# Optimization experiments

Measured on AMD Instinct MI355X. Metric: run time of the kernel, lower is better.

The kernel has to match this reference:

```python
import jax, jax.numpy as jnp
import numpy as np

B, LINES, NREG, D, L, K, CATS = 256, 64, 64, 1024, 64, 16, 2
EPS = 1e-5

_idx = np.arange(K)
# modular digit-wise add / sub mixing tables: M[i,j,m] = 1 iff (i op j) mod K == m
M_ADD = jnp.asarray(((_idx[:, None] + _idx[None, :]) % K)[..., None] == _idx[None, None, :], dtype=jnp.float32)
M_SUB = jnp.asarray(((_idx[:, None] - _idx[None, :]) % K)[..., None] == _idx[None, None, :], dtype=jnp.float32)


def _ln(x, g, b):
    m = x.mean(-1, keepdims=True)
    v = ((x - m) ** 2).mean(-1, keepdims=True)
    return (x - m) / jnp.sqrt(v + EPS) * g + b


def setup_inputs() -> dict:
    key = jax.random.key(0)
    ks = jax.random.split(key, 12)
    p = jax.random.uniform(ks[0], (B, LINES, CATS))
    opcode_probs = p / p.sum(-1, keepdims=True)
    registers = jax.random.normal(ks[1], (B, NREG, D))
    k_write = jax.random.normal(ks[2], (B, LINES, D))
    q_read = jax.random.normal(ks[3], (B, LINES, 2, D))
    cond_distribution = jax.random.uniform(ks[4], (B, LINES, 4))
    gate = jax.random.uniform(ks[5], (B, LINES, 1))
    s = 0.02
    F = L * K
    return {
        'opcode_probs': opcode_probs, 'registers': registers, 'k_write': k_write,
        'q_read': q_read, 'cond_distribution': cond_distribution, 'gate': gate,
        'ln1_g': jnp.ones((D,)), 'ln1_b': jnp.zeros((D,)),
        'w1': jax.random.normal(ks[6], (D, F)) * s, 'b1': jnp.zeros((F,)),
        'ln2_g': jnp.ones((D,)), 'ln2_b': jnp.zeros((D,)),
        'w2': jax.random.normal(ks[7], (D, F)) * s, 'b2': jnp.zeros((F,)),
        'w_res': jax.random.normal(ks[8], (F, D)) * s, 'b_res': jnp.zeros((D,)),
        'lno_g': jnp.ones((D,)), 'lno_b': jnp.zeros((D,)),
    }


def reference(opcode_probs, registers, k_write, q_read, cond_distribution, gate,
              ln1_g, ln1_b, w1, b1, ln2_g, ln2_b, w2, b2, w_res, b_res, lno_g, lno_b):
    scale = 1.0 / jnp.sqrt(jnp.asarray(D, jnp.float32))

    def digit_op(x, y, M):
        # x,y: (b,l,k) digit distributions -> (b,l,k) modular arithmetic result
        return jnp.einsum('bli,blj,ijm->blm', x, y, M)

    def step(R, xs):
        prob, q, kw, g = xs  # (b,2) (b,2,d) (b,d) (b,1)
        # attention read of two operands from register memory
        attn = jax.nn.softmax(jnp.einsum('bqd,brd->bqr', q, R) * scale, axis=-1)
        op_s = jnp.einsum('bqr,brd->bqd', attn, R)
        x = jax.nn.softmax((_ln(op_s[:, 0], ln1_g, ln1_b) @ w1 + b1).reshape(-1, L, K), axis=-1)
        y = jax.nn.softmax((_ln(op_s[:, 1], ln2_g, ln2_b) @ w2 + b2).reshape(-1, L, K), axis=-1)
        outs = jnp.stack([digit_op(x, y, M_ADD), digit_op(x, y, M_SUB)], axis=1)  # (b,2,l,k)
        mix = jnp.einsum('bn,bnlk->blk', prob, outs).reshape(-1, L * K)
        value = _ln(mix @ w_res + b_res, lno_g, lno_b)  # (b,d)
        # attention write-back with gate
        w = jax.nn.softmax(jnp.einsum('bd,brd->br', kw, R) * scale, axis=-1)
        gw = (g * w)[..., None]  # (b,r,1)
        R = R * (1.0 - gw) + gw * value[:, None, :]
        return R, None

    xs = (jnp.moveaxis(opcode_probs, 1, 0), jnp.moveaxis(q_read, 1, 0),
          jnp.moveaxis(k_write, 1, 0), jnp.moveaxis(gate, 1, 0))
    R, _ = jax.lax.scan(step, registers, xs)
    return R
```

## Files before the change

kernel.cpp:

```cpp
#include <hip/hip_runtime.h>
#include <hip/hip_bf16.h>

#define BB 256
#define LINES 64
#define NREG 64
#define DD 1024
#define FF 1024

constexpr float EPS = 1e-5f;
constexpr float SCALE = 0.03125f;

typedef __bf16 bf16_t;
typedef bf16_t bf16x8 __attribute__((ext_vector_type(8)));
typedef unsigned short us16x8 __attribute__((ext_vector_type(8)));
typedef float f32x4 __attribute__((ext_vector_type(4)));
typedef unsigned long long u64;

#define WS_W1T   0u
#define WS_W2T   (2u << 20)
#define WS_WRT   (4u << 20)
#define WS_XNP   (6u << 20)
#define WS_GT    ((7u << 20) + (1u << 19))
#define WS_CTR   ((8u << 20) + (1u << 19))
#define WS_XCDC  (WS_CTR + 1024u)
#define WS_NEED  (WS_XCDC + 64u)

#define SM_WV    0
#define SM_AT0P  256
#define SM_AT1P  512
#define SM_SC0   768
#define SM_SC1   1024
#define SM_SCW   1280
#define SM_RED   1536
#define SM_DYNID 1792
#define SM_DYN   2048
#define SM_OSB   SM_DYN
#define SM_AT0   SM_DYN
#define SM_AT1   (SM_DYN + 32768)
#define SM_RED2  (SM_DYN + 65536)
#define SM_PRE   (SM_DYN + 65536 + 13056)
#define SM_VAL   (SM_DYN + 65536 + 13056 + 8448)
#define SM_QPF   (SM_VAL + 4352)
#define SM_MIXT  (SM_QPF + 15360)
#define SM_SIZE  (SM_MIXT + 2304)

__device__ __forceinline__ float wred(float v) {
#pragma unroll
  for (int m = 32; m >= 1; m >>= 1) v += __shfl_xor(v, m);
  return v;
}
__device__ __forceinline__ float wmax64(float v) {
#pragma unroll
  for (int m = 32; m >= 1; m >>= 1) v = fmaxf(v, __shfl_xor(v, m));
  return v;
}

__device__ __forceinline__ void st_llc32(void* p, unsigned v) {
  asm volatile("global_store_dword %0, %1, off sc0 sc1" :: "v"(p), "v"(v) : "memory");
}
__device__ __forceinline__ unsigned ld_llc32(const void* p) {
  unsigned r;
  asm volatile("global_load_dword %0, %1, off sc0 sc1\n\ts_waitcnt vmcnt(0)"
               : "=v"(r) : "v"(p) : "memory");
  return r;
}
__device__ __forceinline__ void ld_llc_4x8_nw(const void* p, u64& a, u64& b, u64& c, u64& d) {
  asm volatile(
      "global_load_dwordx2 %0, %4, off sc0 sc1\n\t"
      "global_load_dwordx2 %1, %4, off offset:8 sc0 sc1\n\t"
      "global_load_dwordx2 %2, %4, off offset:16 sc0 sc1\n\t"
      "global_load_dwordx2 %3, %4, off offset:24 sc0 sc1"
      : "=&v"(a), "=&v"(b), "=&v"(c), "=&v"(d) : "v"(p) : "memory");
}
__device__ __forceinline__ void wait_vm0() {
  asm volatile("s_waitcnt vmcnt(0)" ::: "memory");
  __builtin_amdgcn_sched_barrier(0);
}

__device__ __forceinline__ void group_barrier(unsigned* flg, int tid, int m, unsigned tag) {
  asm volatile("s_waitcnt vmcnt(0)" ::: "memory");
  __syncthreads();
  if (tid < 64) {
    if (tid == 0) st_llc32(&flg[m], tag);
    for (;;) {
      unsigned v = (tid < 16) ? ld_llc32(&flg[tid]) : tag;
      if (__all(v >= tag)) break;
      __builtin_amdgcn_s_sleep(2);
    }
  }
  __syncthreads();
}

__global__ __launch_bounds__(256) void transcvt(const float* __restrict__ w1,
                                                const float* __restrict__ w2,
                                                const float* __restrict__ wr,
                                                bf16_t* __restrict__ out) {
  __shared__ float tl[64][65];
  const float* src = (blockIdx.z == 0) ? w1 : (blockIdx.z == 1) ? w2 : wr;
  bf16_t* dst = out + (size_t)blockIdx.z * (1u << 20);
  const int i0 = blockIdx.x * 64, j0 = blockIdx.y * 64;
  const int t = threadIdx.x;
#pragma unroll
  for (int it = 0; it < 4; ++it) {
    int r = (t >> 4) + it * 16;
    int c4 = (t & 15) * 4;
    const float4 v = *reinterpret_cast<const float4*>(&src[(size_t)(i0 + r) * 1024 + j0 + c4]);
    tl[r][c4] = v.x; tl[r][c4 + 1] = v.y; tl[r][c4 + 2] = v.z; tl[r][c4 + 3] = v.w;
  }
  __syncthreads();
  const int orow = t >> 2, seg = t & 3;
  bf16x8 v0, v1;
#pragma unroll
  for (int u = 0; u < 8; ++u) {
    v0[u] = (bf16_t)tl[seg * 16 + u][orow];
    v1[u] = (bf16_t)tl[seg * 16 + 8 + u][orow];
  }
  bf16_t* dp = dst + (size_t)(j0 + orow) * 1024 + i0 + seg * 16;
  *reinterpret_cast<bf16x8*>(dp) = v0;
  *reinterpret_cast<bf16x8*>(dp + 8) = v1;
}

__global__ __launch_bounds__(1024, 4) void interp5(
    const float* __restrict__ opcode_probs, const float* __restrict__ Rin,
    const float* __restrict__ k_write, const float* __restrict__ q_read,
    const float* __restrict__ gate,
    const float* __restrict__ ln1_g, const float* __restrict__ ln1_b, const float* __restrict__ b1,
    const float* __restrict__ ln2_g, const float* __restrict__ ln2_b, const float* __restrict__ b2,
    const float* __restrict__ b_res, const float* __restrict__ lno_g, const float* __restrict__ lno_b,
    char* __restrict__ ws, float* __restrict__ Rout) {
  __shared__ __align__(16) char smem[SM_SIZE];
  float* wvp  = (float*)(smem + SM_WV);
  float* at0p = (float*)(smem + SM_AT0P);
  float* at1p = (float*)(smem + SM_AT1P);
  float* sc0p = (float*)(smem + SM_SC0);
  float* sc1p = (float*)(smem + SM_SC1);
  float* scwp = (float*)(smem + SM_SCW);
  float* redp = (float*)(smem + SM_RED);
  int*   dyn  = (int*)(smem + SM_DYNID);

  const int tid = threadIdx.x;
  const int w = tid >> 6, lane = tid & 63;
  const int ln15 = lane & 15, kgrp = lane >> 4;

  if (tid == 0) {
    unsigned x = __builtin_amdgcn_s_getreg(20 | (31 << 11)) & 7;
    unsigned r = atomicAdd((unsigned*)(ws + WS_XCDC) + x, 1u);
    dyn[0] = (int)x; dyn[1] = (int)r;
  }
  __syncthreads();
  const int xcd = dyn[0];
  const int rnk = dyn[1];
  const int g = (rnk >> 1) & 15;
  const int m = ((xcd << 1) | (rnk & 1)) & 15;
  const int j = m;
  const int bq = g * 16 + j;

  const bf16_t* w1t = (const bf16_t*)(ws + WS_W1T);
  const bf16_t* w2t = (const bf16_t*)(ws + WS_W2T);
  const bf16_t* wrt = (const bf16_t*)(ws + WS_WRT);
  unsigned* xnp   = (unsigned*)(ws + WS_XNP);
  float*    gtf   = (float*)(ws + WS_GT);
  unsigned* gtu   = (unsigned*)(ws + WS_GT);
  unsigned* flg   = (unsigned*)(ws + WS_CTR) + g * 16;

  float Rr_[4][16];
  {
    const float* Rsrc = Rin + (size_t)bq * (NREG * DD);
#pragma unroll
    for (int rr = 0; rr < 4; ++rr) {
#pragma unroll
      for (int c = 0; c < 4; ++c) {
        float4 v = *(const float4*)(Rsrc + (size_t)(4 * w + rr) * DD + lane * 16 + c * 4);
        Rr_[rr][c * 4 + 0] = v.x; Rr_[rr][c * 4 + 1] = v.y;
        Rr_[rr][c * 4 + 2] = v.z; Rr_[rr][c * 4 + 3] = v.w;
      }
    }
  }

  {
    const float* qb = q_read + ((size_t)bq * LINES + 0) * (2 * DD);
    const float* kb = k_write + ((size_t)bq * LINES + 0) * DD;
    float* qpf = (float*)(smem + SM_QPF);
    const int pidx = (tid >> 4) * 20 + (tid & 15);
    qpf[pidx] = qb[tid];
    qpf[1280 + pidx] = qb[DD + tid];
    qpf[2560 + pidx] = kb[tid];
  }
  __syncthreads();

  unsigned nbar = 0;

  for (int t = 0; t < LINES; ++t) {
    {
      const float* qpf = (const float*)(smem + SM_QPF);
      const int pb = lane * 20;
#pragma unroll
      for (int v = 0; v < 3; ++v) {
        float* dst = (v == 0) ? sc0p : (v == 1) ? sc1p : scwp;
        float qv[16];
#pragma unroll
        for (int c = 0; c < 4; ++c) {
          float4 t4 = *(const float4*)(qpf + v * 1280 + pb + c * 4);
          qv[c * 4 + 0] = t4.x; qv[c * 4 + 1] = t4.y;
          qv[c * 4 + 2] = t4.z; qv[c * 4 + 3] = t4.w;
        }
#pragma unroll
        for (int rr = 0; rr < 4; ++rr) {
          float s = 0.f;
#pragma unroll
          for (int jj = 0; jj < 16; ++jj) s = fmaf(Rr_[rr][jj], qv[jj], s);
          s = wred(s);
          if (lane == 0) dst[4 * w + rr] = s * SCALE;
        }
      }
    }
    __syncthreads();
    if (w < 3) {
      const float* src = (w == 0) ? sc0p : (w == 1) ? sc1p : scwp;
      float* dst = (w == 0) ? at0p : (w == 1) ? at1p : wvp;
      float v = src[lane];
      float mx = wmax64(v);
      float e = expf(v - mx);
      float s = wred(e);
      dst[lane] = e / s;
    }
    float pf0, pf1, pf2;
    {
      int tn = (t + 1 < LINES) ? (t + 1) : (LINES - 1);
      const float* qb2 = q_read + ((size_t)bq * LINES + tn) * (2 * DD);
      const float* kb2 = k_write + ((size_t)bq * LINES + tn) * DD;
      pf0 = qb2[tid]; pf1 = qb2[DD + tid]; pf2 = kb2[tid];
    }
    __syncthreads();
    float os0, os1;
    {
      float p0[16], p1[16];
#pragma unroll
      for (int jj = 0; jj < 16; ++jj) { p0[jj] = 0.f; p1[jj] = 0.f; }
#pragma unroll
      for (int rr = 0; rr < 4; ++rr) {
        float a0 = at0p[4 * w + rr], a1 = at1p[4 * w + rr];
#pragma unroll
        for (int jj = 0; jj < 16; ++jj) {
          p0[jj] = fmaf(a0, Rr_[rr][jj], p0[jj]);
          p1[jj] = fmaf(a1, Rr_[rr][jj], p1[jj]);
        }
      }
      float* osb = (float*)(smem + SM_OSB);
      const int rp = (tid >> 4) * 17 + (tid & 15);
#pragma unroll
      for (int jj = 0; jj < 16; ++jj) osb[w * 1088 + lane * 17 + jj] = p0[jj];
      __syncthreads();
      os0 = 0.f;
#pragma unroll
      for (int ww = 0; ww < 16; ++ww) os0 += osb[ww * 1088 + rp];
      __syncthreads();
#pragma unroll
      for (int jj = 0; jj < 16; ++jj) osb[w * 1088 + lane * 17 + jj] = p1[jj];
      __syncthreads();
      os1 = 0.f;
#pragma unroll
      for (int ww = 0; ww < 16; ++ww) os1 += osb[ww * 1088 + rp];
    }
    {
      float s0 = wred(os0), qq0 = wred(os0 * os0);
      float s1 = wred(os1), qq1 = wred(os1 * os1);
      if (lane == 0) { redp[w*4] = s0; redp[w*4+1] = qq0; redp[w*4+2] = s1; redp[w*4+3] = qq1; }
      __syncthreads();
      float S0 = 0, Q0 = 0, S1 = 0, Q1 = 0;
#pragma unroll
      for (int i = 0; i < 16; ++i) { S0 += redp[i*4]; Q0 += redp[i*4+1]; S1 += redp[i*4+2]; Q1 += redp[i*4+3]; }
      float m0 = S0 * (1.f / DD), v0 = fmaxf(Q0 * (1.f / DD) - m0 * m0, 0.f);
      float m1 = S1 * (1.f / DD), v1 = fmaxf(Q1 * (1.f / DD) - m1 * m1, 0.f);
      float xn0v = (os0 - m0) * rsqrtf(v0 + EPS) * ln1_g[tid] + ln1_b[tid];
      float xn1v = (os1 - m1) * rsqrtf(v1 + EPS) * ln2_g[tid] + ln2_b[tid];
      unsigned pw = (unsigned)__builtin_bit_cast(unsigned short, (bf16_t)xn0v)
                  | ((unsigned)__builtin_bit_cast(unsigned short, (bf16_t)xn1v) << 16);
      st_llc32(&xnp[((size_t)g * 16 + j) * DD + tid], pw);
    }
    group_barrier(flg, tid, m, ++nbar);

    {
      const char* base = (const char*)(xnp + (size_t)g * (16 * DD));
      const int row = tid >> 7, k16 = tid & 127;
      u64 a0, a1, a2, a3, c0, c1, c2, c3;
      ld_llc_4x8_nw(base + (size_t)row * 4096 + k16 * 32, a0, a1, a2, a3);
      ld_llc_4x8_nw(base + (size_t)(row + 8) * 4096 + k16 * 32, c0, c1, c2, c3);
      wait_vm0();
#pragma unroll
      for (int h = 0; h < 2; ++h) {
        u64 x0 = h ? c0 : a0, x1 = h ? c1 : a1, x2 = h ? c2 : a2, x3 = h ? c3 : a3;
        int r = row + h * 8;
        us16x8 v0, v1;
        v0[0] = (unsigned short)x0;         v1[0] = (unsigned short)(x0 >> 16);
        v0[1] = (unsigned short)(x0 >> 32); v1[1] = (unsigned short)(x0 >> 48);
        v0[2] = (unsigned short)x1;         v1[2] = (unsigned short)(x1 >> 16);
        v0[3] = (unsigned short)(x1 >> 32); v1[3] = (unsigned short)(x1 >> 48);
        v0[4] = (unsigned short)x2;         v1[4] = (unsigned short)(x2 >> 16);
        v0[5] = (unsigned short)(x2 >> 32); v1[5] = (unsigned short)(x2 >> 48);
        v0[6] = (unsigned short)x3;         v1[6] = (unsigned short)(x3 >> 16);
        v0[7] = (unsigned short)(x3 >> 32); v1[7] = (unsigned short)(x3 >> 48);
        unsigned byte = (unsigned)(r * 2048 + k16 * 16) ^ ((unsigned)(r & 7) << 4);
        *(us16x8*)(smem + SM_AT0 + byte) = v0;
        *(us16x8*)(smem + SM_AT1 + byte) = v1;
      }
    }
    __syncthreads();

#pragma unroll
    for (int gm = 0; gm < 2; ++gm) {
      const char* atile = smem + (gm ? SM_AT1 : SM_AT0);
      const int ns = w & 3, ks = w >> 2;
      const bf16_t* bsrc = (gm ? w2t : w1t) + (size_t)(64 * m + ns * 16 + ln15) * DD;
      f32x4 acc = {0.f, 0.f, 0.f, 0.f};
#pragma unroll
      for (int kc = 0; kc < 8; ++kc) {
        int kb = ks * 256 + kc * 32 + kgrp * 8;
        unsigned abyte = ((unsigned)(ln15 * 2048 + kb * 2)) ^ ((unsigned)(ln15 & 7) << 4);
        bf16x8 av = *(const bf16x8*)(atile + abyte);
        bf16x8 bv = *(const bf16x8*)(bsrc + kb);
        acc = __builtin_amdgcn_mfma_f32_16x16x32_bf16(av, bv, acc, 0, 0, 0);
      }
      float* red2 = (float*)(smem + SM_RED2);
      if (ks > 0) {
#pragma unroll
        for (int r2 = 0; r2 < 4; ++r2)
          red2[((ks - 1) * 4 + ns) * (16 * 17) + (kgrp * 4 + r2) * 17 + ln15] = acc[r2];
      }
      __syncthreads();
      if (ks == 0) {
        float* prep = (float*)(smem + SM_PRE) + gm * (16 * 66);
#pragma unroll
        for (int r2 = 0; r2 < 4; ++r2) {
          int crow = kgrp * 4 + r2;
          float v = acc[r2];
#pragma unroll
          for (int kk = 0; kk < 3; ++kk)
            v += red2[(kk * 4 + ns) * (16 * 17) + crow * 17 + ln15];
          prep[crow * 66 + ns * 16 + ln15] = v;
        }
      }
      __syncthreads();
    }
    {
      float* prep = (float*)(smem + SM_PRE);
      const int bb2 = w, c = lane;
      float xp = prep[bb2 * 66 + c] + b1[64 * m + c];
      float yp = prep[16 * 66 + bb2 * 66 + c] + b2[64 * m + c];
      float mx1 = xp, mx2 = yp;
#pragma unroll
      for (int msk = 1; msk < 16; msk <<= 1) {
        mx1 = fmaxf(mx1, __shfl_xor(mx1, msk));
        mx2 = fmaxf(mx2, __shfl_xor(mx2, msk));
      }
      float e1 = expf(xp - mx1), e2 = expf(yp - mx2);
      float s1 = e1, s2 = e2;
#pragma unroll
      for (int msk = 1; msk < 16; msk <<= 1) {
        s1 += __shfl_xor(s1, msk);
        s2 += __shfl_xor(s2, msk);
      }
      float x = e1 / s1, y = e2 / s2;
      int mm = lane & 15, basel = lane & ~15;
      float addv = 0.f, subv = 0.f;
#pragma unroll
      for (int i = 0; i < 16; ++i) {
        float xi = __shfl(x, basel + i);
        float ya = __shfl(y, basel + ((mm - i) & 15));
        float ys = __shfl(y, basel + ((i - mm) & 15));
        addv = fmaf(xi, ya, addv);
        subv = fmaf(xi, ys, subv);
      }
      int q2 = g * 16 + bb2;
      const float* pr = opcode_probs + ((size_t)q2 * LINES + t) * 2;
      float mix = pr[0] * addv + pr[1] * subv;
      ((bf16_t*)(smem + SM_MIXT))[bb2 * 72 + c] = (bf16_t)mix;
    }
    __syncthreads();

    {
      const bf16_t* mixT = (const bf16_t*)(smem + SM_MIXT);
      f32x4 acc[4] = {{0.f,0.f,0.f,0.f},{0.f,0.f,0.f,0.f},{0.f,0.f,0.f,0.f},{0.f,0.f,0.f,0.f}};
#pragma unroll
      for (int ks2 = 0; ks2 < 2; ++ks2) {
        int fk = ks2 * 32 + kgrp * 8;
        bf16x8 av = *(const bf16x8*)(mixT + ln15 * 72 + fk);
#pragma unroll
        for (int nt2 = 0; nt2 < 4; ++nt2) {
          int d = 64 * w + nt2 * 16 + ln15;
          const bf16_t* bp = wrt + (size_t)d * DD + 64 * m + fk;
          bf16x8 bv = *(const bf16x8*)bp;
          acc[nt2] = __builtin_amdgcn_mfma_f32_16x16x32_bf16(av, bv, acc[nt2], 0, 0, 0);
        }
      }
#pragma unroll
      for (int nt2 = 0; nt2 < 4; ++nt2) {
        int d = 64 * w + nt2 * 16 + ln15;
#pragma unroll
        for (int r2 = 0; r2 < 4; ++r2) {
          int crow = kgrp * 4 + r2;
          atomicAdd(&gtf[((size_t)g * 16 + crow) * DD + d], acc[nt2][r2]);
        }
      }
    }
    group_barrier(flg, tid, m, ++nbar);

    {
      float xv = __builtin_bit_cast(float, ld_llc32(&gtu[((size_t)g * 16 + j) * DD + tid]))
               + b_res[tid];
      st_llc32(&gtu[((size_t)g * 16 + j) * DD + tid], 0u);
      float s1 = wred(xv), s2 = wred(xv * xv);
      if (lane == 0) { redp[w * 2] = s1; redp[w * 2 + 1] = s2; }
      __syncthreads();
      float S = 0.f, Q = 0.f;
#pragma unroll
      for (int i = 0; i < 16; ++i) { S += redp[i * 2]; Q += redp[i * 2 + 1]; }
      float mn = S * (1.f / DD), vr = fmaxf(Q * (1.f / DD) - mn * mn, 0.f);
      float vv = (xv - mn) * rsqrtf(vr + EPS) * lno_g[tid] + lno_b[tid];
      float* valp = (float*)(smem + SM_VAL);
      valp[(tid >> 4) * 17 + (tid & 15)] = vv;
    }
    __syncthreads();
    {
      float gtv = gate[(size_t)bq * LINES + t];
      const float* valp = (const float*)(smem + SM_VAL);
      float vvj[16];
#pragma unroll
      for (int jj = 0; jj < 16; ++jj) vvj[jj] = valp[lane * 17 + jj];
#pragma unroll
      for (int rr = 0; rr < 4; ++rr) {
        float gg = gtv * wvp[4 * w + rr];
#pragma unroll
        for (int jj = 0; jj < 16; ++jj)
          Rr_[rr][jj] = Rr_[rr][jj] * (1.f - gg) + gg * vvj[jj];
      }
      float* qpf = (float*)(smem + SM_QPF);
      const int pidx = (tid >> 4) * 20 + (tid & 15);
      qpf[pidx] = pf0;
      qpf[1280 + pidx] = pf1;
      qpf[2560 + pidx] = pf2;
    }
    __syncthreads();
  }

  {
    float* Rdst = Rout + (size_t)bq * (NREG * DD);
#pragma unroll
    for (int rr = 0; rr < 4; ++rr) {
#pragma unroll
      for (int c = 0; c < 4; ++c) {
        float4 v;
        v.x = Rr_[rr][c * 4 + 0]; v.y = Rr_[rr][c * 4 + 1];
        v.z = Rr_[rr][c * 4 + 2]; v.w = Rr_[rr][c * 4 + 3];
        *(float4*)(Rdst + (size_t)(4 * w + rr) * DD + lane * 16 + c * 4) = v;
      }
    }
  }
}

__global__ __launch_bounds__(1024) void interp_fb(
    const float* __restrict__ opcode_probs, const float* __restrict__ k_write,
    const float* __restrict__ q_read, const float* __restrict__ gate,
    const float* __restrict__ ln1_g, const float* __restrict__ ln1_b,
    const float* __restrict__ w1, const float* __restrict__ b1,
    const float* __restrict__ ln2_g, const float* __restrict__ ln2_b,
    const float* __restrict__ w2, const float* __restrict__ b2,
    const float* __restrict__ w_res, const float* __restrict__ b_res,
    const float* __restrict__ lno_g, const float* __restrict__ lno_b,
    float* __restrict__ R) {
  __shared__ float q0s[DD], q1s[DD], kws[DD];
  __shared__ float sc0[NREG], sc1[NREG], scw[NREG];
  __shared__ float at0[NREG], at1[NREG], wv[NREG];
  __shared__ float xn0[DD], xn1[DD];
  __shared__ float mixs[FF];
  __shared__ float val[DD];
  __shared__ float red[64];
  const int b = blockIdx.x;
  const int tid = threadIdx.x;
  const int w = tid >> 6, lane = tid & 63;
  float* Rb = R + (size_t)b * NREG * DD;
  for (int t = 0; t < LINES; ++t) {
    const float* qb = q_read + ((size_t)b * LINES + t) * 2 * DD;
    const float* kb = k_write + ((size_t)b * LINES + t) * DD;
    q0s[tid] = qb[tid]; q1s[tid] = qb[DD + tid]; kws[tid] = kb[tid];
    __syncthreads();
#pragma unroll
    for (int rr = 0; rr < 4; ++rr) {
      int r = w * 4 + rr;
      const float* Rr = Rb + (size_t)r * DD;
      float a0 = 0.f, a1 = 0.f, aw = 0.f;
#pragma unroll
      for (int jj = 0; jj < 16; ++jj) {
        int d = jj * 64 + lane;
        float rv = Rr[d];
        a0 += rv * q0s[d]; a1 += rv * q1s[d]; aw += rv * kws[d];
      }
      a0 = wred(a0); a1 = wred(a1); aw = wred(aw);
      if (lane == 0) { sc0[r] = a0 * SCALE; sc1[r] = a1 * SCALE; scw[r] = aw * SCALE; }
    }
    __syncthreads();
    if (w < 3) {
      const float* src = (w == 0) ? sc0 : (w == 1) ? sc1 : scw;
      float* dst = (w == 0) ? at0 : (w == 1) ? at1 : wv;
      float v = src[lane];
      float mx = wmax64(v);
      float e = expf(v - mx);
      float s = wred(e);
      dst[lane] = e / s;
    }
    __syncthreads();
    float os0 = 0.f, os1 = 0.f;
#pragma unroll 4
    for (int r = 0; r < NREG; ++r) {
      float rv = Rb[(size_t)r * DD + tid];
      os0 += at0[r] * rv; os1 += at1[r] * rv;
    }
    {
      float s0 = wred(os0), qq0 = wred(os0 * os0);
      float s1 = wred(os1), qq1 = wred(os1 * os1);
      if (lane == 0) { red[w*4] = s0; red[w*4+1] = qq0; red[w*4+2] = s1; red[w*4+3] = qq1; }
      __syncthreads();
      float S0 = 0, Q0 = 0, S1 = 0, Q1 = 0;
#pragma unroll
      for (int i = 0; i < 16; ++i) { S0 += red[i*4]; Q0 += red[i*4+1]; S1 += red[i*4+2]; Q1 += red[i*4+3]; }
      float m0 = S0 / DD, v0 = fmaxf(Q0 / DD - m0 * m0, 0.f);
      float m1 = S1 / DD, v1 = fmaxf(Q1 / DD - m1 * m1, 0.f);
      xn0[tid] = (os0 - m0) * rsqrtf(v0 + EPS) * ln1_g[tid] + ln1_b[tid];
      xn1[tid] = (os1 - m1) * rsqrtf(v1 + EPS) * ln2_g[tid] + ln2_b[tid];
      __syncthreads();
    }
    float p1v = b1[tid], p2v = b2[tid];
    {
      const float* c1 = w1 + tid;
      const float* c2 = w2 + tid;
#pragma unroll 4
      for (int d = 0; d < DD; ++d) {
        p1v += xn0[d] * c1[(size_t)d * FF];
        p2v += xn1[d] * c2[(size_t)d * FF];
      }
    }
    {
      int mmm = lane & 15, basel = lane & ~15;
      float mx1 = p1v, mx2 = p2v;
      for (int msk = 1; msk < 16; msk <<= 1) {
        mx1 = fmaxf(mx1, __shfl_xor(mx1, msk));
        mx2 = fmaxf(mx2, __shfl_xor(mx2, msk));
      }
      float e1 = expf(p1v - mx1), e2 = expf(p2v - mx2);
      float s1 = e1, s2 = e2;
      for (int msk = 1; msk < 16; msk <<= 1) { s1 += __shfl_xor(s1, msk); s2 += __shfl_xor(s2, msk); }
      float x = e1 / s1, y = e2 / s2;
      float addv = 0.f, subv = 0.f;
#pragma unroll
      for (int i = 0; i < 16; ++i) {
        float xi = __shfl(x, basel + i);
        float ya = __shfl(y, basel + ((mmm - i) & 15));
        float ys = __shfl(y, basel + ((i - mmm) & 15));
        addv += xi * ya; subv += xi * ys;
      }
      const float* pr = opcode_probs + ((size_t)b * LINES + t) * 2;
      mixs[tid] = pr[0] * addv + pr[1] * subv;
    }
    __syncthreads();
    float acc = b_res[tid];
    {
      const float* cr = w_res + tid;
#pragma unroll 4
      for (int f = 0; f < FF; ++f) acc += mixs[f] * cr[(size_t)f * DD];
    }
    {
      float s1 = wred(acc), s2 = wred(acc * acc);
      if (lane == 0) { red[w*2] = s1; red[w*2+1] = s2; }
      __syncthreads();
      float S = 0, Q = 0;
#pragma unroll
      for (int i = 0; i < 16; ++i) { S += red[i*2]; Q += red[i*2+1]; }
      float mn = S / DD, vr = fmaxf(Q / DD - mn * mn, 0.f);
      val[tid] = (acc - mn) * rsqrtf(vr + EPS) * lno_g[tid] + lno_b[tid];
      __syncthreads();
    }
    {
      float gt_ = gate[(size_t)b * LINES + t];
      float vv = val[tid];
#pragma unroll 4
      for (int r = 0; r < NREG; ++r) {
        float gg = gt_ * wv[r];
        size_t idx = (size_t)r * DD + tid;
        Rb[idx] = Rb[idx] * (1.f - gg) + gg * vv;
      }
    }
    __syncthreads();
  }
}

extern "C" void kernel_launch(void* const* d_in, const int* in_sizes, int n_in,
                              void* d_out, int out_size, void* d_ws, size_t ws_size,
                              hipStream_t stream) {
  const float* opcode = (const float*)d_in[0];
  const float* registers = (const float*)d_in[1];
  const float* k_write = (const float*)d_in[2];
  const float* q_read = (const float*)d_in[3];
  const float* gate = (const float*)d_in[5];
  const float* ln1_g = (const float*)d_in[6];
  const float* ln1_b = (const float*)d_in[7];
  const float* w1 = (const float*)d_in[8];
  const float* b1 = (const float*)d_in[9];
  const float* ln2_g = (const float*)d_in[10];
  const float* ln2_b = (const float*)d_in[11];
  const float* w2 = (const float*)d_in[12];
  const float* b2 = (const float*)d_in[13];
  const float* w_res = (const float*)d_in[14];
  const float* b_res = (const float*)d_in[15];
  const float* lno_g = (const float*)d_in[16];
  const float* lno_b = (const float*)d_in[17];
  float* R = (float*)d_out;

  if (ws_size >= (size_t)WS_NEED) {
    transcvt<<<dim3(16, 16, 3), 256, 0, stream>>>(w1, w2, w_res, (bf16_t*)d_ws);
    hipMemsetAsync((char*)d_ws + WS_GT, 0, (1u << 20) + 2048, stream);
    interp5<<<BB, 1024, 0, stream>>>(opcode, registers, k_write, q_read, gate,
                                     ln1_g, ln1_b, b1, ln2_g, ln2_b, b2,
                                     b_res, lno_g, lno_b, (char*)d_ws, R);
  } else {
    hipMemcpyAsync(R, registers, (size_t)BB * NREG * DD * sizeof(float),
                   hipMemcpyDeviceToDevice, stream);
    interp_fb<<<BB, 1024, 0, stream>>>(opcode, k_write, q_read, gate, ln1_g, ln1_b,
                                       w1, b1, ln2_g, ln2_b, w2, b2, w_res, b_res,
                                       lno_g, lno_b, R);
  }
}
```

Measured before the change: 4.126 ms.

## Precompute next-step attention scores before barrier and apply write-back algebraically

The per-step q·R and k·R score dot products now run on the pre-update registers, placed before the group barrier so they overlap the wait. The scores are then corrected algebraically for the gated write-back, using the dot products of q and k with the new value vector and the previous gate weights. The block-to-batch mapping also drops the XCD-based atomic rank assignment in favour of blockIdx directly. This adds a few extra reductions and reorders floating-point arithmetic, and it changes which blocks share the L2-coherent group barrier.

Result: no change. 4.088 ms (-0.9%).

```diff
diff --git a/kernel.cpp b/kernel.cpp
--- a/kernel.cpp
+++ b/kernel.cpp
@@ -22,17 +22,16 @@
 #define WS_XNP   (6u << 20)
 #define WS_GT    ((7u << 20) + (1u << 19))
 #define WS_CTR   ((8u << 20) + (1u << 19))
-#define WS_XCDC  (WS_CTR + 1024u)
-#define WS_NEED  (WS_XCDC + 64u)
+#define WS_NEED  (WS_CTR + 1024u)
 
 #define SM_WV    0
 #define SM_AT0P  256
 #define SM_AT1P  512
-#define SM_SC0   768
-#define SM_SC1   1024
-#define SM_SCW   1280
+#define SM_PC0   768
+#define SM_PC1   1024
+#define SM_PCW   1280
 #define SM_RED   1536
-#define SM_DYNID 1792
+#define SM_VQG   1856
 #define SM_DYN   2048
 #define SM_OSB   SM_DYN
 #define SM_AT0   SM_DYN
@@ -77,11 +76,11 @@
   __builtin_amdgcn_sched_barrier(0);
 }
 
-__device__ __forceinline__ void group_barrier(unsigned* flg, int tid, int m, unsigned tag) {
+__device__ __forceinline__ void group_barrier(unsigned* flg, int tid, int me, unsigned tag) {
   asm volatile("s_waitcnt vmcnt(0)" ::: "memory");
   __syncthreads();
   if (tid < 64) {
-    if (tid == 0) st_llc32(&flg[m], tag);
+    if (tid == 0) st_llc32(&flg[me], tag);
     for (;;) {
       unsigned v = (tid < 16) ? ld_llc32(&flg[tid]) : tag;
       if (__all(v >= tag)) break;
@@ -120,7 +119,7 @@
   *reinterpret_cast<bf16x8*>(dp + 8) = v1;
 }
 
-__global__ __launch_bounds__(1024, 4) void interp5(
+__global__ __launch_bounds__(1024, 4) void interp6(
     const float* __restrict__ opcode_probs, const float* __restrict__ Rin,
     const float* __restrict__ k_write, const float* __restrict__ q_read,
     const float* __restrict__ gate,
@@ -132,28 +131,21 @@
   float* wvp  = (float*)(smem + SM_WV);
   float* at0p = (float*)(smem + SM_AT0P);
   float* at1p = (float*)(smem + SM_AT1P);
-  float* sc0p = (float*)(smem + SM_SC0);
-  float* sc1p = (float*)(smem + SM_SC1);
-  float* scwp = (float*)(smem + SM_SCW);
+  float* pc0  = (float*)(smem + SM_PC0);
+  float* pc1  = (float*)(smem + SM_PC1);
+  float* pcw  = (float*)(smem + SM_PCW);
   float* redp = (float*)(smem + SM_RED);
-  int*   dyn  = (int*)(smem + SM_DYNID);
+  float* vqg  = (float*)(smem + SM_VQG);
 
   const int tid = threadIdx.x;
   const int w = tid >> 6, lane = tid & 63;
   const int ln15 = lane & 15, kgrp = lane >> 4;
 
-  if (tid == 0) {
-    unsigned x = __builtin_amdgcn_s_getreg(20 | (31 << 11)) & 7;
-    unsigned r = atomicAdd((unsigned*)(ws + WS_XCDC) + x, 1u);
-    dyn[0] = (int)x; dyn[1] = (int)r;
-  }
-  __syncthreads();
-  const int xcd = dyn[0];
-  const int rnk = dyn[1];
-  const int g = (rnk >> 1) & 15;
-  const int m = ((xcd << 1) | (rnk & 1)) & 15;
-  const int j = m;
-  const int bq = g * 16 + j;
+  const int b = blockIdx.x;
+  const int g = b >> 4;
+  const int j = b & 15;
+  const int m = ((b & 7) << 1) | ((b >> 3) & 1);
+  const int bq = b;
 
   const bf16_t* w1t = (const bf16_t*)(ws + WS_W1T);
   const bf16_t* w2t = (const bf16_t*)(ws + WS_W2T);
@@ -185,40 +177,43 @@
     qpf[pidx] = qb[tid];
     qpf[1280 + pidx] = qb[DD + tid];
     qpf[2560 + pidx] = kb[tid];
+    if (tid < 64) wvp[tid] = 0.f;
+    if (tid < 4) vqg[tid] = 0.f;
   }
   __syncthreads();
+  {
+    const float* qpf = (const float*)(smem + SM_QPF);
+    const int pb = lane * 20;
+#pragma unroll
+    for (int v = 0; v < 3; ++v) {
+      float* dst = (v == 0) ? pc0 : (v == 1) ? pc1 : pcw;
+      float qv[16];
+#pragma unroll
+      for (int c = 0; c < 4; ++c) {
+        float4 t4 = *(const float4*)(qpf + v * 1280 + pb + c * 4);
+        qv[c * 4 + 0] = t4.x; qv[c * 4 + 1] = t4.y;
+        qv[c * 4 + 2] = t4.z; qv[c * 4 + 3] = t4.w;
+      }
+#pragma unroll
+      for (int rr = 0; rr < 4; ++rr) {
+        float s = 0.f;
+#pragma unroll
+        for (int jj = 0; jj < 16; ++jj) s = fmaf(Rr_[rr][jj], qv[jj], s);
+        s = wred(s);
+        if (lane == 0) dst[4 * w + rr] = s;
+      }
+    }
+  }
+  __syncthreads();
 
   unsigned nbar = 0;
 
   for (int t = 0; t < LINES; ++t) {
-    {
-      const float* qpf = (const float*)(smem + SM_QPF);
-      const int pb = lane * 20;
-#pragma unroll
-      for (int v = 0; v < 3; ++v) {
-        float* dst = (v == 0) ? sc0p : (v == 1) ? sc1p : scwp;
-        float qv[16];
-#pragma unroll
-        for (int c = 0; c < 4; ++c) {
-          float4 t4 = *(const float4*)(qpf + v * 1280 + pb + c * 4);
-          qv[c * 4 + 0] = t4.x; qv[c * 4 + 1] = t4.y;
-          qv[c * 4 + 2] = t4.z; qv[c * 4 + 3] = t4.w;
-        }
-#pragma unroll
-        for (int rr = 0; rr < 4; ++rr) {
-          float s = 0.f;
-#pragma unroll
-          for (int jj = 0; jj < 16; ++jj) s = fmaf(Rr_[rr][jj], qv[jj], s);
-          s = wred(s);
-          if (lane == 0) dst[4 * w + rr] = s * SCALE;
-        }
-      }
-    }
-    __syncthreads();
     if (w < 3) {
-      const float* src = (w == 0) ? sc0p : (w == 1) ? sc1p : scwp;
+      const float* P = (w == 0) ? pc0 : (w == 1) ? pc1 : pcw;
       float* dst = (w == 0) ? at0p : (w == 1) ? at1p : wvp;
-      float v = src[lane];
+      float gw = vqg[3] * wvp[lane];
+      float v = ((1.f - gw) * P[lane] + gw * vqg[w]) * SCALE;
       float mx = wmax64(v);
       float e = expf(v - mx);
       float s = wred(e);
@@ -278,7 +273,7 @@
                   | ((unsigned)__builtin_bit_cast(unsigned short, (bf16_t)xn1v) << 16);
       st_llc32(&xnp[((size_t)g * 16 + j) * DD + tid], pw);
     }
-    group_barrier(flg, tid, m, ++nbar);
+    group_barrier(flg, tid, j, ++nbar);
 
     {
       const char* base = (const char*)(xnp + (size_t)g * (16 * DD));
@@ -403,42 +398,81 @@
         }
       }
     }
-    group_barrier(flg, tid, m, ++nbar);
-
-    {
-      float xv = __builtin_bit_cast(float, ld_llc32(&gtu[((size_t)g * 16 + j) * DD + tid]))
-               + b_res[tid];
-      st_llc32(&gtu[((size_t)g * 16 + j) * DD + tid], 0u);
-      float s1 = wred(xv), s2 = wred(xv * xv);
-      if (lane == 0) { redp[w * 2] = s1; redp[w * 2 + 1] = s2; }
-      __syncthreads();
-      float S = 0.f, Q = 0.f;
-#pragma unroll
-      for (int i = 0; i < 16; ++i) { S += redp[i * 2]; Q += redp[i * 2 + 1]; }
-      float mn = S * (1.f / DD), vr = fmaxf(Q * (1.f / DD) - mn * mn, 0.f);
-      float vv = (xv - mn) * rsqrtf(vr + EPS) * lno_g[tid] + lno_b[tid];
-      float* valp = (float*)(smem + SM_VAL);
-      valp[(tid >> 4) * 17 + (tid & 15)] = vv;
-    }
-    __syncthreads();
-    {
-      float gtv = gate[(size_t)bq * LINES + t];
-      const float* valp = (const float*)(smem + SM_VAL);
-      float vvj[16];
-#pragma unroll
-      for (int jj = 0; jj < 16; ++jj) vvj[jj] = valp[lane * 17 + jj];
-#pragma unroll
-      for (int rr = 0; rr < 4; ++rr) {
-        float gg = gtv * wvp[4 * w + rr];
-#pragma unroll
-        for (int jj = 0; jj < 16; ++jj)
-          Rr_[rr][jj] = Rr_[rr][jj] * (1.f - gg) + gg * vvj[jj];
-      }
+    {
       float* qpf = (float*)(smem + SM_QPF);
       const int pidx = (tid >> 4) * 20 + (tid & 15);
       qpf[pidx] = pf0;
       qpf[1280 + pidx] = pf1;
       qpf[2560 + pidx] = pf2;
+    }
+    __syncthreads();
+    {
+      const float* qpf = (const float*)(smem + SM_QPF);
+      const int pb = lane * 20;
+#pragma unroll
+      for (int v = 0; v < 3; ++v) {
+        float* dst = (v == 0) ? pc0 : (v == 1) ? pc1 : pcw;
+        float qv[16];
+#pragma unroll
+        for (int c = 0; c < 4; ++c) {
+          float4 t4 = *(const float4*)(qpf + v * 1280 + pb + c * 4);
+          qv[c * 4 + 0] = t4.x; qv[c * 4 + 1] = t4.y;
+          qv[c * 4 + 2] = t4.z; qv[c * 4 + 3] = t4.w;
+        }
+#pragma unroll
+        for (int rr = 0; rr < 4; ++rr) {
+          float s = 0.f;
+#pragma unroll
+          for (int jj = 0; jj < 16; ++jj) s = fmaf(Rr_[rr][jj], qv[jj], s);
+          s = wred(s);
+          if (lane == 0) dst[4 * w + rr] = s;
+        }
+      }
+    }
+    group_barrier(flg, tid, j, ++nbar);
+
+    {
+      float xv = __builtin_bit_cast(float, ld_llc32(&gtu[((size_t)g * 16 + j) * DD + tid]))
+               + b_res[tid];
+      st_llc32(&gtu[((size_t)g * 16 + j) * DD + tid], 0u);
+      float s1 = wred(xv), s2 = wred(xv * xv);
+      if (lane == 0) { redp[w * 5] = s1; redp[w * 5 + 1] = s2; }
+      __syncthreads();
+      float S = 0.f, Q = 0.f;
+#pragma unroll
+      for (int i = 0; i < 16; ++i) { S += redp[i * 5]; Q += redp[i * 5 + 1]; }
+      float mn = S * (1.f / DD), vr = fmaxf(Q * (1.f / DD) - mn * mn, 0.f);
+      float vv = (xv - mn) * rsqrtf(vr + EPS) * lno_g[tid] + lno_b[tid];
+      float* valp = (float*)(smem + SM_VAL);
+      valp[(tid >> 4) * 17 + (tid & 15)] = vv;
+      const float* qpf = (const float*)(smem + SM_QPF);
+      const int pidx = (tid >> 4) * 20 + (tid & 15);
+      float t0 = wred(vv * qpf[pidx]);
+      float t1 = wred(vv * qpf[1280 + pidx]);
+      float t2 = wred(vv * qpf[2560 + pidx]);
+      if (lane == 0) { redp[w * 5 + 2] = t0; redp[w * 5 + 3] = t1; redp[w * 5 + 4] = t2; }
+    }
+    __syncthreads();
+    {
+      float gtv = gate[(size_t)bq * LINES + t];
+      const float* valp = (const float*)(smem + SM_VAL);
+      float vvj[16];
+#pragma unroll
+      for (int jj = 0; jj < 16; ++jj) vvj[jj] = valp[lane * 17 + jj];
+#pragma unroll
+      for (int rr = 0; rr < 4; ++rr) {
+        float gg = gtv * wvp[4 * w + rr];
+#pragma unroll
+        for (int jj = 0; jj < 16; ++jj)
+          Rr_[rr][jj] = Rr_[rr][jj] * (1.f - gg) + gg * vvj[jj];
+      }
+      if (tid < 3) {
+        float s = 0.f;
+#pragma unroll
+        for (int i = 0; i < 16; ++i) s += redp[i * 5 + 2 + tid];
+        vqg[tid] = s;
+      }
+      if (tid == 3) vqg[3] = gtv;
     }
     __syncthreads();
   }
@@ -617,8 +651,8 @@
 
   if (ws_size >= (size_t)WS_NEED) {
     transcvt<<<dim3(16, 16, 3), 256, 0, stream>>>(w1, w2, w_res, (bf16_t*)d_ws);
-    hipMemsetAsync((char*)d_ws + WS_GT, 0, (1u << 20) + 2048, stream);
-    interp5<<<BB, 1024, 0, stream>>>(opcode, registers, k_write, q_read, gate,
+    hipMemsetAsync((char*)d_ws + WS_GT, 0, (1u << 20) + 1024, stream);
+    interp6<<<BB, 1024, 0, stream>>>(opcode, registers, k_write, q_read, gate,
                                      ln1_g, ln1_b, b1, ln2_g, ln2_b, b2,
                                      b_res, lno_g, lno_b, (char*)d_ws, R);
   } else {
```

## Shrink cooperative groups to 4 blocks on one XCD with L2-scoped exchange

Applied to the files above, without the earlier changes.

Cooperating groups of workgroups shrink from 16 blocks to 4 blocks, and each group now sits entirely on one XCD. Each block computes a 256-column slice of the F dimension instead of 64. Because a group no longer spans XCDs, the activation exchange uses sc0 (L2-scope) loads and stores instead of sc0 sc1 system-coherent ones. The fp32 atomicAdd reduction of the residual projection is replaced with bf16 partial stores that each block sums after the barrier, which also removes the zeroing memset. The goal is cheaper cross-block synchronisation and less LLC traffic, at the cost of more per-block GEMM work, lower-precision partial sums, and a reliance on the XCD placement assumption for coherence.

Result: slower. 5.298 ms (+28.4%).

```diff
diff --git a/kernel.cpp b/kernel.cpp
--- a/kernel.cpp
+++ b/kernel.cpp
@@ -20,9 +20,9 @@
 #define WS_W2T   (2u << 20)
 #define WS_WRT   (4u << 20)
 #define WS_XNP   (6u << 20)
-#define WS_GT    ((7u << 20) + (1u << 19))
-#define WS_CTR   ((8u << 20) + (1u << 19))
-#define WS_XCDC  (WS_CTR + 1024u)
+#define WS_PGT   (7u << 20)
+#define WS_CTR   (9u << 20)
+#define WS_XCDC  ((9u << 20) + 1024u)
 #define WS_NEED  (WS_XCDC + 64u)
 
 #define SM_WV    0
@@ -37,12 +37,11 @@
 #define SM_OSB   SM_DYN
 #define SM_AT0   SM_DYN
 #define SM_AT1   (SM_DYN + 32768)
-#define SM_RED2  (SM_DYN + 65536)
-#define SM_PRE   (SM_DYN + 65536 + 13056)
-#define SM_VAL   (SM_DYN + 65536 + 13056 + 8448)
+#define SM_PREP  (SM_DYN + 69632)
+#define SM_MIXT  (SM_PREP + 8448)
+#define SM_VAL   (SM_MIXT + 2112)
 #define SM_QPF   (SM_VAL + 4352)
-#define SM_MIXT  (SM_QPF + 15360)
-#define SM_SIZE  (SM_MIXT + 2304)
+#define SM_SIZE  (SM_QPF + 15360)
 
 __device__ __forceinline__ float wred(float v) {
 #pragma unroll
@@ -64,26 +63,46 @@
                : "=v"(r) : "v"(p) : "memory");
   return r;
 }
-__device__ __forceinline__ void ld_llc_4x8_nw(const void* p, u64& a, u64& b, u64& c, u64& d) {
+
+__device__ __forceinline__ void st_l232(void* p, unsigned v) {
+  asm volatile("global_store_dword %0, %1, off sc0" :: "v"(p), "v"(v) : "memory");
+}
+__device__ __forceinline__ void st_l216b(void* p, unsigned short v) {
+  unsigned vv = v;
+  asm volatile("global_store_short %0, %1, off sc0" :: "v"(p), "v"(vv) : "memory");
+}
+__device__ __forceinline__ void ld_l2_4x8_nw(const void* p, u64& a, u64& b, u64& c, u64& d) {
   asm volatile(
-      "global_load_dwordx2 %0, %4, off sc0 sc1\n\t"
-      "global_load_dwordx2 %1, %4, off offset:8 sc0 sc1\n\t"
-      "global_load_dwordx2 %2, %4, off offset:16 sc0 sc1\n\t"
-      "global_load_dwordx2 %3, %4, off offset:24 sc0 sc1"
+      "global_load_dwordx2 %0, %4, off sc0\n\t"
+      "global_load_dwordx2 %1, %4, off offset:8 sc0\n\t"
+      "global_load_dwordx2 %2, %4, off offset:16 sc0\n\t"
+      "global_load_dwordx2 %3, %4, off offset:24 sc0"
       : "=&v"(a), "=&v"(b), "=&v"(c), "=&v"(d) : "v"(p) : "memory");
+}
+__device__ __forceinline__ void ld_l2_u16x4_nw(const void* p0, const void* p1,
+                                               const void* p2, const void* p3,
+                                               unsigned& a, unsigned& b,
+                                               unsigned& c, unsigned& d) {
+  asm volatile(
+      "global_load_ushort %0, %4, off sc0\n\t"
+      "global_load_ushort %1, %5, off sc0\n\t"
+      "global_load_ushort %2, %6, off sc0\n\t"
+      "global_load_ushort %3, %7, off sc0"
+      : "=&v"(a), "=&v"(b), "=&v"(c), "=&v"(d)
+      : "v"(p0), "v"(p1), "v"(p2), "v"(p3) : "memory");
 }
 __device__ __forceinline__ void wait_vm0() {
   asm volatile("s_waitcnt vmcnt(0)" ::: "memory");
   __builtin_amdgcn_sched_barrier(0);
 }
 
-__device__ __forceinline__ void group_barrier(unsigned* flg, int tid, int m, unsigned tag) {
+__device__ __forceinline__ void group_barrier(unsigned* flg, int tid, int me, unsigned tag) {
   asm volatile("s_waitcnt vmcnt(0)" ::: "memory");
   __syncthreads();
   if (tid < 64) {
-    if (tid == 0) st_llc32(&flg[m], tag);
+    if (tid == 0) st_llc32(&flg[me], tag);
     for (;;) {
-      unsigned v = (tid < 16) ? ld_llc32(&flg[tid]) : tag;
+      unsigned v = (tid < 4) ? ld_llc32(&flg[tid]) : tag;
       if (__all(v >= tag)) break;
       __builtin_amdgcn_s_sleep(2);
     }
@@ -120,7 +139,7 @@
   *reinterpret_cast<bf16x8*>(dp + 8) = v1;
 }
 
-__global__ __launch_bounds__(1024, 4) void interp5(
+__global__ __launch_bounds__(1024, 4) void interp7(
     const float* __restrict__ opcode_probs, const float* __restrict__ Rin,
     const float* __restrict__ k_write, const float* __restrict__ q_read,
     const float* __restrict__ gate,
@@ -149,19 +168,17 @@
   }
   __syncthreads();
   const int xcd = dyn[0];
-  const int rnk = dyn[1];
-  const int g = (rnk >> 1) & 15;
-  const int m = ((xcd << 1) | (rnk & 1)) & 15;
-  const int j = m;
-  const int bq = g * 16 + j;
+  const int rnk = dyn[1] & 31;
+  const int g = xcd * 8 + (rnk >> 2);
+  const int m4 = rnk & 3;
+  const int bq = g * 4 + m4;
 
   const bf16_t* w1t = (const bf16_t*)(ws + WS_W1T);
   const bf16_t* w2t = (const bf16_t*)(ws + WS_W2T);
   const bf16_t* wrt = (const bf16_t*)(ws + WS_WRT);
-  unsigned* xnp   = (unsigned*)(ws + WS_XNP);
-  float*    gtf   = (float*)(ws + WS_GT);
-  unsigned* gtu   = (unsigned*)(ws + WS_GT);
-  unsigned* flg   = (unsigned*)(ws + WS_CTR) + g * 16;
+  unsigned* xnp = (unsigned*)(ws + WS_XNP);
+  bf16_t*   pgt = (bf16_t*)(ws + WS_PGT);
+  unsigned* flg = (unsigned*)(ws + WS_CTR) + g * 4;
 
   float Rr_[4][16];
   {
@@ -276,77 +293,59 @@
       float xn1v = (os1 - m1) * rsqrtf(v1 + EPS) * ln2_g[tid] + ln2_b[tid];
       unsigned pw = (unsigned)__builtin_bit_cast(unsigned short, (bf16_t)xn0v)
                   | ((unsigned)__builtin_bit_cast(unsigned short, (bf16_t)xn1v) << 16);
-      st_llc32(&xnp[((size_t)g * 16 + j) * DD + tid], pw);
-    }
-    group_barrier(flg, tid, m, ++nbar);
-
-    {
-      const char* base = (const char*)(xnp + (size_t)g * (16 * DD));
+      st_l232(&xnp[((size_t)g * 4 + m4) * DD + tid], pw);
+    }
+    group_barrier(flg, tid, m4, ++nbar);
+
+    if (tid < 512) {
+      const char* base = (const char*)(xnp + (size_t)g * (4 * DD));
       const int row = tid >> 7, k16 = tid & 127;
-      u64 a0, a1, a2, a3, c0, c1, c2, c3;
-      ld_llc_4x8_nw(base + (size_t)row * 4096 + k16 * 32, a0, a1, a2, a3);
-      ld_llc_4x8_nw(base + (size_t)(row + 8) * 4096 + k16 * 32, c0, c1, c2, c3);
+      u64 a0, a1, a2, a3;
+      ld_l2_4x8_nw(base + (size_t)row * 4096 + k16 * 32, a0, a1, a2, a3);
       wait_vm0();
-#pragma unroll
-      for (int h = 0; h < 2; ++h) {
-        u64 x0 = h ? c0 : a0, x1 = h ? c1 : a1, x2 = h ? c2 : a2, x3 = h ? c3 : a3;
-        int r = row + h * 8;
-        us16x8 v0, v1;
-        v0[0] = (unsigned short)x0;         v1[0] = (unsigned short)(x0 >> 16);
-        v0[1] = (unsigned short)(x0 >> 32); v1[1] = (unsigned short)(x0 >> 48);
-        v0[2] = (unsigned short)x1;         v1[2] = (unsigned short)(x1 >> 16);
-        v0[3] = (unsigned short)(x1 >> 32); v1[3] = (unsigned short)(x1 >> 48);
-        v0[4] = (unsigned short)x2;         v1[4] = (unsigned short)(x2 >> 16);
-        v0[5] = (unsigned short)(x2 >> 32); v1[5] = (unsigned short)(x2 >> 48);
-        v0[6] = (unsigned short)x3;         v1[6] = (unsigned short)(x3 >> 16);
-        v0[7] = (unsigned short)(x3 >> 32); v1[7] = (unsigned short)(x3 >> 48);
-        unsigned byte = (unsigned)(r * 2048 + k16 * 16) ^ ((unsigned)(r & 7) << 4);
-        *(us16x8*)(smem + SM_AT0 + byte) = v0;
-        *(us16x8*)(smem + SM_AT1 + byte) = v1;
-      }
-    }
-    __syncthreads();
-
-#pragma unroll
-    for (int gm = 0; gm < 2; ++gm) {
-      const char* atile = smem + (gm ? SM_AT1 : SM_AT0);
-      const int ns = w & 3, ks = w >> 2;
-      const bf16_t* bsrc = (gm ? w2t : w1t) + (size_t)(64 * m + ns * 16 + ln15) * DD;
-      f32x4 acc = {0.f, 0.f, 0.f, 0.f};
-#pragma unroll
-      for (int kc = 0; kc < 8; ++kc) {
-        int kb = ks * 256 + kc * 32 + kgrp * 8;
-        unsigned abyte = ((unsigned)(ln15 * 2048 + kb * 2)) ^ ((unsigned)(ln15 & 7) << 4);
-        bf16x8 av = *(const bf16x8*)(atile + abyte);
-        bf16x8 bv = *(const bf16x8*)(bsrc + kb);
-        acc = __builtin_amdgcn_mfma_f32_16x16x32_bf16(av, bv, acc, 0, 0, 0);
-      }
-      float* red2 = (float*)(smem + SM_RED2);
-      if (ks > 0) {
-#pragma unroll
-        for (int r2 = 0; r2 < 4; ++r2)
-          red2[((ks - 1) * 4 + ns) * (16 * 17) + (kgrp * 4 + r2) * 17 + ln15] = acc[r2];
-      }
-      __syncthreads();
-      if (ks == 0) {
-        float* prep = (float*)(smem + SM_PRE) + gm * (16 * 66);
-#pragma unroll
-        for (int r2 = 0; r2 < 4; ++r2) {
-          int crow = kgrp * 4 + r2;
-          float v = acc[r2];
-#pragma unroll
-          for (int kk = 0; kk < 3; ++kk)
-            v += red2[(kk * 4 + ns) * (16 * 17) + crow * 17 + ln15];
-          prep[crow * 66 + ns * 16 + ln15] = v;
+      us16x8 v0, v1;
+      v0[0] = (unsigned short)a0;         v1[0] = (unsigned short)(a0 >> 16);
+      v0[1] = (unsigned short)(a0 >> 32); v1[1] = (unsigned short)(a0 >> 48);
+      v0[2] = (unsigned short)a1;         v1[2] = (unsigned short)(a1 >> 16);
+      v0[3] = (unsigned short)(a1 >> 32); v1[3] = (unsigned short)(a1 >> 48);
+      v0[4] = (unsigned short)a2;         v1[4] = (unsigned short)(a2 >> 16);
+      v0[5] = (unsigned short)(a2 >> 32); v1[5] = (unsigned short)(a2 >> 48);
+      v0[6] = (unsigned short)a3;         v1[6] = (unsigned short)(a3 >> 16);
+      v0[7] = (unsigned short)(a3 >> 32); v1[7] = (unsigned short)(a3 >> 48);
+      unsigned byte = (unsigned)(row * 2048 + k16 * 16) ^ ((unsigned)(row & 7) << 4);
+      *(us16x8*)(smem + SM_AT0 + byte) = v0;
+      *(us16x8*)(smem + SM_AT1 + byte) = v1;
+    }
+    __syncthreads();
+
+    {
+      float* prep = (float*)(smem + SM_PREP);
+#pragma unroll
+      for (int gm = 0; gm < 2; ++gm) {
+        const char* atile = smem + (gm ? SM_AT1 : SM_AT0);
+        const bf16_t* bsrc = (gm ? w2t : w1t) + (size_t)(m4 * 256 + w * 16 + ln15) * DD;
+        f32x4 acc = {0.f, 0.f, 0.f, 0.f};
+#pragma unroll 8
+        for (int kc = 0; kc < 32; ++kc) {
+          int kb = kc * 32 + kgrp * 8;
+          unsigned abyte = ((unsigned)(ln15 * 2048 + kb * 2)) ^ ((unsigned)(ln15 & 7) << 4);
+          bf16x8 av = *(const bf16x8*)(atile + abyte);
+          bf16x8 bv = *(const bf16x8*)(bsrc + kb);
+          acc = __builtin_amdgcn_mfma_f32_16x16x32_bf16(av, bv, acc, 0, 0, 0);
         }
-      }
-      __syncthreads();
-    }
-    {
-      float* prep = (float*)(smem + SM_PRE);
-      const int bb2 = w, c = lane;
-      float xp = prep[bb2 * 66 + c] + b1[64 * m + c];
-      float yp = prep[16 * 66 + bb2 * 66 + c] + b2[64 * m + c];
+        if (kgrp == 0) {
+#pragma unroll
+          for (int r2 = 0; r2 < 4; ++r2)
+            prep[(gm * 4 + r2) * 264 + w * 16 + ln15] = acc[r2];
+        }
+      }
+    }
+    __syncthreads();
+    {
+      const float* prep = (const float*)(smem + SM_PREP);
+      const int bb2 = tid >> 8, c = tid & 255;
+      float xp = prep[(0 * 4 + bb2) * 264 + c] + b1[m4 * 256 + c];
+      float yp = prep[(1 * 4 + bb2) * 264 + c] + b2[m4 * 256 + c];
       float mx1 = xp, mx2 = yp;
 #pragma unroll
       for (int msk = 1; msk < 16; msk <<= 1) {
@@ -371,10 +370,10 @@
         addv = fmaf(xi, ya, addv);
         subv = fmaf(xi, ys, subv);
       }
-      int q2 = g * 16 + bb2;
+      int q2 = g * 4 + bb2;
       const float* pr = opcode_probs + ((size_t)q2 * LINES + t) * 2;
       float mix = pr[0] * addv + pr[1] * subv;
-      ((bf16_t*)(smem + SM_MIXT))[bb2 * 72 + c] = (bf16_t)mix;
+      ((bf16_t*)(smem + SM_MIXT))[bb2 * 264 + c] = (bf16_t)mix;
     }
     __syncthreads();
 
@@ -382,33 +381,38 @@
       const bf16_t* mixT = (const bf16_t*)(smem + SM_MIXT);
       f32x4 acc[4] = {{0.f,0.f,0.f,0.f},{0.f,0.f,0.f,0.f},{0.f,0.f,0.f,0.f},{0.f,0.f,0.f,0.f}};
 #pragma unroll
-      for (int ks2 = 0; ks2 < 2; ++ks2) {
-        int fk = ks2 * 32 + kgrp * 8;
-        bf16x8 av = *(const bf16x8*)(mixT + ln15 * 72 + fk);
+      for (int kc2 = 0; kc2 < 8; ++kc2) {
+        int fk = kc2 * 32 + kgrp * 8;
+        bf16x8 av = *(const bf16x8*)(mixT + ln15 * 264 + fk);
 #pragma unroll
         for (int nt2 = 0; nt2 < 4; ++nt2) {
-          int d = 64 * w + nt2 * 16 + ln15;
-          const bf16_t* bp = wrt + (size_t)d * DD + 64 * m + fk;
+          int d = w * 64 + nt2 * 16 + ln15;
+          const bf16_t* bp = wrt + (size_t)d * DD + m4 * 256 + fk;
           bf16x8 bv = *(const bf16x8*)bp;
           acc[nt2] = __builtin_amdgcn_mfma_f32_16x16x32_bf16(av, bv, acc[nt2], 0, 0, 0);
         }
       }
-#pragma unroll
-      for (int nt2 = 0; nt2 < 4; ++nt2) {
-        int d = 64 * w + nt2 * 16 + ln15;
-#pragma unroll
-        for (int r2 = 0; r2 < 4; ++r2) {
-          int crow = kgrp * 4 + r2;
-          atomicAdd(&gtf[((size_t)g * 16 + crow) * DD + d], acc[nt2][r2]);
+      if (kgrp == 0) {
+#pragma unroll
+        for (int nt2 = 0; nt2 < 4; ++nt2) {
+          int d = w * 64 + nt2 * 16 + ln15;
+#pragma unroll
+          for (int r2 = 0; r2 < 4; ++r2)
+            st_l216b(&pgt[(((size_t)g * 4 + m4) * 4 + r2) * DD + d],
+                     __builtin_bit_cast(unsigned short, (bf16_t)acc[nt2][r2]));
         }
       }
     }
-    group_barrier(flg, tid, m, ++nbar);
-
-    {
-      float xv = __builtin_bit_cast(float, ld_llc32(&gtu[((size_t)g * 16 + j) * DD + tid]))
+    group_barrier(flg, tid, m4, ++nbar);
+
+    {
+      const bf16_t* base = pgt + ((size_t)g * 16 + m4) * DD + tid;
+      unsigned r0, r1, r2u, r3u;
+      ld_l2_u16x4_nw(base, base + 4 * DD, base + 8 * DD, base + 12 * DD, r0, r1, r2u, r3u);
+      wait_vm0();
+      float xv = __builtin_bit_cast(float, r0 << 16) + __builtin_bit_cast(float, r1 << 16)
+               + __builtin_bit_cast(float, r2u << 16) + __builtin_bit_cast(float, r3u << 16)
                + b_res[tid];
-      st_llc32(&gtu[((size_t)g * 16 + j) * DD + tid], 0u);
       float s1 = wred(xv), s2 = wred(xv * xv);
       if (lane == 0) { redp[w * 2] = s1; redp[w * 2 + 1] = s2; }
       __syncthreads();
@@ -617,8 +621,8 @@
 
   if (ws_size >= (size_t)WS_NEED) {
     transcvt<<<dim3(16, 16, 3), 256, 0, stream>>>(w1, w2, w_res, (bf16_t*)d_ws);
-    hipMemsetAsync((char*)d_ws + WS_GT, 0, (1u << 20) + 2048, stream);
-    interp5<<<BB, 1024, 0, stream>>>(opcode, registers, k_write, q_read, gate,
+    hipMemsetAsync((char*)d_ws + WS_CTR, 0, 2048, stream);
+    interp7<<<BB, 1024, 0, stream>>>(opcode, registers, k_write, q_read, gate,
                                      ln1_g, ln1_b, b1, ln2_g, ln2_b, b2,
                                      b_res, lno_g, lno_b, (char*)d_ws, R);
   } else {
```
